# Kernel tuning notes

Hardware: AMD Instinct MI355X
Metric: run time of the kernel (lower is better)

## Reference

```python
import jax, jax.numpy as jnp
import numpy as np

N = 50000
E = 1600000
IN_DIM = 128
HID = 32
CLS = 40
HEADS = [4, 4, 1]
SLOPE = 0.2


def gat_conv(x, W, al, ar, src, dst, activation):
    # x: [N, F_in], W: [F_in, H*D], al/ar: [H, D]
    H, D = al.shape
    f = (x @ W).reshape(N, H, D)                       # projected features [N,H,D]
    el = jnp.sum(f * al, axis=-1)                      # [N,H]
    er = jnp.sum(f * ar, axis=-1)                      # [N,H]
    e = jax.nn.leaky_relu(el[src] + er[dst], SLOPE)    # [E,H] raw attention logits
    m = jax.ops.segment_max(e, dst, num_segments=N)    # per-dst max for stability
    m = jnp.where(jnp.isfinite(m), m, 0.0)
    ee = jnp.exp(e - m[dst])                           # [E,H]
    s = jax.ops.segment_sum(ee, dst, num_segments=N)   # [N,H]
    alpha = ee / s[dst]                                # edge softmax over in-neighbors
    out = jax.ops.segment_sum(alpha[..., None] * f[src], dst, num_segments=N)  # [N,H,D]
    if activation:
        out = jax.nn.elu(out)
    return out


def setup_inputs() -> dict:
    key = jax.random.key(0)
    ks = jax.random.split(key, 12)
    inputs = jax.random.normal(ks[0], (N, IN_DIM), dtype=jnp.float32)
    # random edges + self-loops so every node has >=1 in-edge
    src = jax.random.randint(ks[1], (E - N,), 0, N)
    dst = jax.random.randint(ks[2], (E - N,), 0, N)
    loops = jnp.arange(N)
    src = jnp.concatenate([src, loops])
    dst = jnp.concatenate([dst, loops])

    def glorot(k, shape):
        fan = shape[0] + shape[-1] * (shape[1] if len(shape) == 3 else 1)
        return jax.random.normal(k, shape, dtype=jnp.float32) * np.sqrt(2.0 / fan)

    W0 = glorot(ks[3], (IN_DIM, HEADS[0] * HID))
    al0 = jax.random.normal(ks[4], (HEADS[0], HID), dtype=jnp.float32) * 0.1
    ar0 = jax.random.normal(ks[5], (HEADS[0], HID), dtype=jnp.float32) * 0.1
    W1 = glorot(ks[6], (HEADS[0] * HID, HEADS[1] * HID))
    al1 = jax.random.normal(ks[7], (HEADS[1], HID), dtype=jnp.float32) * 0.1
    ar1 = jax.random.normal(ks[8], (HEADS[1], HID), dtype=jnp.float32) * 0.1
    W2 = glorot(ks[9], (HEADS[1] * HID, HEADS[2] * CLS))
    al2 = jax.random.normal(ks[10], (HEADS[2], CLS), dtype=jnp.float32) * 0.1
    ar2 = jax.random.normal(ks[11], (HEADS[2], CLS), dtype=jnp.float32) * 0.1
    return {"inputs": inputs, "src": src, "dst": dst,
            "W0": W0, "al0": al0, "ar0": ar0,
            "W1": W1, "al1": al1, "ar1": ar1,
            "W2": W2, "al2": al2, "ar2": ar2}


def reference(inputs, src, dst, W0, al0, ar0, W1, al1, ar1, W2, al2, ar2):
    h = gat_conv(inputs, W0, al0, ar0, src, dst, True).reshape(N, -1)   # flatten heads
    h = gat_conv(h, W1, al1, ar1, src, dst, True).reshape(N, -1)
    logits = gat_conv(h, W2, al2, ar2, src, dst, False).mean(axis=1)    # [N, CLS]
    return jax.nn.log_softmax(logits, axis=-1), h
```

## Files before the change

kernel.cpp:

```cpp
#include <hip/hip_runtime.h>
#include <hip/hip_fp16.h>
#include <math.h>

#define NN 50000
#define EE 1600000
#define DEGPAD 96
#define NWIN 200
#define WINSZ 250
#define WCAP 8960
#define BLDT 512
#define AGG_WPB 4

typedef _Float16 f16x8 __attribute__((ext_vector_type(8)));
typedef _Float16 f16x4v __attribute__((ext_vector_type(4)));
typedef _Float16 f16x2 __attribute__((ext_vector_type(2)));
typedef float f32x4 __attribute__((ext_vector_type(4)));
typedef float f32x2 __attribute__((ext_vector_type(2)));


__global__ void csr_clear(int* __restrict__ bcnt) {
    int i = blockIdx.x * blockDim.x + threadIdx.x;
    if (i < NWIN) bcnt[i] = 0;
}

__global__ void edge_bucket(const int* __restrict__ src, const int* __restrict__ dst,
                            int* __restrict__ bcnt, unsigned int* __restrict__ buck) {
    __shared__ int lcnt[NWIN];
    __shared__ int lbase[NWIN];
    int t = threadIdx.x;
    for (int i = t; i < NWIN; i += 256) lcnt[i] = 0;
    __syncthreads();
    unsigned int packs[8]; short wins[8]; short ranks[8];
    int e0 = blockIdx.x * 2048;
    #pragma unroll
    for (int it = 0; it < 8; ++it) {
        int e = e0 + it * 256 + t;
        wins[it] = -1;
        if (e < EE) {
            int d = dst[e], s = src[e];
            int w = d / WINSZ;
            wins[it] = (short)w;
            packs[it] = ((unsigned int)d << 16) | (unsigned int)s;
            ranks[it] = (short)atomicAdd(&lcnt[w], 1);
        }
    }
    __syncthreads();
    for (int i = t; i < NWIN; i += 256) lbase[i] = atomicAdd(&bcnt[i], lcnt[i]);
    __syncthreads();
    #pragma unroll
    for (int it = 0; it < 8; ++it) {
        if (wins[it] >= 0)
            buck[(int)wins[it] * WCAP + lbase[wins[it]] + (int)ranks[it]] = packs[it];
    }
}

__global__ void csr_build(const unsigned int* __restrict__ buck, const int* __restrict__ bcnt,
                          int* __restrict__ deg, unsigned short* __restrict__ csr16) {
    __shared__ unsigned short lcsr[WINSZ * DEGPAD];
    __shared__ int ldeg[WINSZ];
    int w = blockIdx.x;
    int n0 = w * WINSZ;
    int t = threadIdx.x;
    for (int i = t; i < WINSZ; i += BLDT) ldeg[i] = 0;
    __syncthreads();
    int cnt = bcnt[w];
    const unsigned int* b = buck + (size_t)w * WCAP;
    for (int i = t; i < cnt; i += BLDT) {
        unsigned int p = b[i];
        int d = (int)(p >> 16) - n0;
        int r = atomicAdd(&ldeg[d], 1);
        lcsr[d * DEGPAD + r] = (unsigned short)(p & 0xffffu);
    }
    __syncthreads();
    const int4* s4 = (const int4*)lcsr;
    int4* d4 = (int4*)(csr16 + (size_t)n0 * DEGPAD);
    for (int i = t; i < WINSZ * DEGPAD * 2 / 16; i += BLDT) d4[i] = s4[i];
    for (int i = t; i < WINSZ; i += BLDT) deg[n0 + i] = ldeg[i];
}


__global__ void cast_x(const float* __restrict__ x, _Float16* __restrict__ y) {
    int i = blockIdx.x * blockDim.x + threadIdx.x;
    if (i >= NN * 32) return;
    float4 v = ((const float4*)x)[i];
    f16x4v o;
    o.x = (_Float16)v.x; o.y = (_Float16)v.y; o.z = (_Float16)v.z; o.w = (_Float16)v.w;
    ((f16x4v*)y)[i] = o;
}

template<int CT, int CPAD, int CREAL, int HH, int CTPH, int F8>
__global__ void proj_mfma(const _Float16* __restrict__ x, const float* __restrict__ W,
                          const float* __restrict__ al, const float* __restrict__ ar,
                          void* __restrict__ fout, float* __restrict__ el,
                          float* __restrict__ er) {
    __shared__ _Float16 wl[4][CT][64][8];
    int lane = threadIdx.x & 63;
    int wave = threadIdx.x >> 6;
    int mrow = blockIdx.x * 64 + wave * 16;

    for (int slot = threadIdx.x; slot < 4 * CT * 64; slot += 256) {
        int lane_s = slot & 63;
        int ct = (slot >> 6) % CT;
        int ks = (slot >> 6) / CT;
        int k0 = ks * 32 + ((lane_s >> 4) << 3);
        int c = ct * 16 + (lane_s & 15);
        f16x8 v;
        #pragma unroll
        for (int j = 0; j < 8; ++j) {
            float w = (c < CREAL) ? W[(k0 + j) * CREAL + c] : 0.0f;
            v[j] = (_Float16)w;
        }
        *(f16x8*)(&wl[ks][ct][lane_s][0]) = v;
    }
    __syncthreads();

    const _Float16* xrow = x + (size_t)(mrow + (lane & 15)) * 128 + ((lane >> 4) << 3);
    f16x8 a[4];
    #pragma unroll
    for (int ks = 0; ks < 4; ++ks) a[ks] = *(const f16x8*)(xrow + ks * 32);

    f32x4 acc[CT];
    #pragma unroll
    for (int ct = 0; ct < CT; ++ct) acc[ct] = (f32x4){0.f, 0.f, 0.f, 0.f};

    #pragma unroll
    for (int ct = 0; ct < CT; ++ct) {
        #pragma unroll
        for (int ks = 0; ks < 4; ++ks) {
            f16x8 b = *(const f16x8*)(&wl[ks][ct][lane][0]);
            acc[ct] = __builtin_amdgcn_mfma_f32_16x16x32_f16(a[ks], b, acc[ct], 0, 0, 0);
        }
    }

    int colb = lane & 15;
    int rowg = lane >> 4;

    #pragma unroll
    for (int ct = 0; ct < CT; ++ct) {
        int c = ct * 16 + colb;
        #pragma unroll
        for (int j = 0; j < 4; ++j) {
            int r = rowg * 4 + j;
            if (F8) {
                int pk = __builtin_amdgcn_cvt_pk_fp8_f32(acc[ct][j], 0.0f, 0, false);
                ((unsigned char*)fout)[(size_t)(mrow + r) * CPAD + c] = (unsigned char)pk;
            } else {
                ((_Float16*)fout)[(size_t)(mrow + r) * CPAD + c] = (_Float16)acc[ct][j];
            }
        }
    }

    #pragma unroll
    for (int h = 0; h < HH; ++h) {
        float pl[4] = {0.f, 0.f, 0.f, 0.f};
        float pr[4] = {0.f, 0.f, 0.f, 0.f};
        #pragma unroll
        for (int q = 0; q < CTPH; ++q) {
            int ct = h * CTPH + q;
            int c = ct * 16 + colb;
            float av = (c < CREAL) ? al[c] : 0.0f;
            float rv = (c < CREAL) ? ar[c] : 0.0f;
            #pragma unroll
            for (int j = 0; j < 4; ++j) { pl[j] += acc[ct][j] * av; pr[j] += acc[ct][j] * rv; }
        }
        #pragma unroll
        for (int m = 1; m < 16; m <<= 1) {
            #pragma unroll
            for (int j = 0; j < 4; ++j) {
                pl[j] += __shfl_xor(pl[j], m);
                pr[j] += __shfl_xor(pr[j], m);
            }
        }
        if (colb == 0) {
            #pragma unroll
            for (int j = 0; j < 4; ++j) {
                int r = rowg * 4 + j;
                el[(size_t)(mrow + r) * HH + h] = pl[j];
                er[(size_t)(mrow + r) * HH + h] = pr[j];
            }
        }
    }
}

__global__ void agg128_kernel(const int* __restrict__ deg, const unsigned short* __restrict__ csr16,
                              const float* __restrict__ el, const float* __restrict__ er,
                              const unsigned char* __restrict__ f8, _Float16* __restrict__ out16,
                              float* __restrict__ out32) {
    __shared__ float ebuf_all[AGG_WPB][16][8];
    int wid  = threadIdx.x >> 6;
    int lane = threadIdx.x & 63;
    int n = blockIdx.x * AGG_WPB + wid;
    if (n >= NN) return;
    float (*ebuf)[8] = ebuf_all[wid];

    int start = n * DEGPAD, end = start + deg[n];
    int slot = lane >> 2, hh = lane & 3;
    int h = lane >> 4;
    float erh = er[n * 4 + hh];
    float acc0 = 0.f, acc1 = 0.f, s_part = 0.f;
    const unsigned char* fbase = f8 + (lane << 1);

    for (int base = start; base < end; base += 16) {
        int cnt = end - base; if (cnt > 16) cnt = 16;
        float eev = 0.0f; int snv = 0;
        if (slot < cnt) {
            snv = csr16[base + slot];
            float v = el[snv * 4 + hh] + erh;
            v = v > 0.0f ? v : 0.2f * v;
            eev = __expf(v);
        }
        s_part += eev;
        asm volatile("s_waitcnt lgkmcnt(0)" ::: "memory");
        ebuf[slot][2 * hh]     = eev;
        ebuf[slot][2 * hh + 1] = __int_as_float(snv);
        asm volatile("s_waitcnt lgkmcnt(0)" ::: "memory");
        #pragma unroll
        for (int g = 0; g < 2; ++g) {
            float ee[8]; int sn[8];
            #pragma unroll
            for (int q = 0; q < 8; ++q) {
                float2 p = *(const float2*)&ebuf[g * 8 + q][2 * h];
                ee[q] = p.x; sn[q] = __float_as_int(p.y);
            }
            unsigned short raw[8];
            #pragma unroll
            for (int q = 0; q < 8; ++q)
                raw[q] = *(const unsigned short*)(fbase + ((size_t)sn[q] << 7));
            #pragma unroll
            for (int q = 0; q < 8; ++q) {
                f32x2 fv = __builtin_amdgcn_cvt_pk_f32_fp8((int)raw[q], false);
                acc0 += ee[q] * fv[0];
                acc1 += ee[q] * fv[1];
            }
        }
    }
    #pragma unroll
    for (int m = 4; m < 64; m <<= 1) s_part += __shfl_xor(s_part, m);
    float sacc = __shfl(s_part, h);

    float o0 = acc0 / sacc, o1 = acc1 / sacc;
    float e0 = o0 > 0.f ? o0 : expm1f(o0);
    float e1 = o1 > 0.f ? o1 : expm1f(o1);
    f16x2 st; st[0] = (_Float16)e0; st[1] = (_Float16)e1;
    *(f16x2*)(out16 + (size_t)n * 128 + (lane << 1)) = st;
    if (out32) {
        float2 s2; s2.x = e0; s2.y = e1;
        *(float2*)(out32 + (size_t)n * 128 + (lane << 1)) = s2;
    }
}

__global__ void agg40_logsm_kernel(const int* __restrict__ deg, const unsigned short* __restrict__ csr16,
                                   const float* __restrict__ el, const float* __restrict__ er,
                                   const __half* __restrict__ f, float* __restrict__ out) {
    int n = blockIdx.x;
    int t = threadIdx.x;
    int start = n * DEGPAD, end = start + deg[n];
    float ern = er[n];
    __shared__ float eebuf[64];
    __shared__ int snbuf[64];

    float acc = 0.0f, sacc = 0.0f;
    for (int base = start; base < end; base += 64) {
        int cnt = end - base;
        if (cnt > 64) cnt = 64;
        if (t < cnt) {
            int sn = csr16[base + t];
            snbuf[t] = sn;
            float v = el[sn] + ern;
            v = v > 0.0f ? v : 0.2f * v;
            eebuf[t] = __expf(v);
        }
        __syncthreads();
        int j = 0;
        for (; j + 8 <= cnt; j += 8) {
            float ee[8]; int sn[8]; float fv[8];
            #pragma unroll
            for (int q = 0; q < 8; ++q) { ee[q] = eebuf[j + q]; sn[q] = snbuf[j + q]; }
            if (t < 40) {
                #pragma unroll
                for (int q = 0; q < 8; ++q) fv[q] = __half2float(f[((size_t)sn[q] << 6) + t]);
                #pragma unroll
                for (int q = 0; q < 8; ++q) acc += ee[q] * fv[q];
            }
            #pragma unroll
            for (int q = 0; q < 8; ++q) sacc += ee[q];
        }
        for (; j < cnt; ++j) {
            float ee = eebuf[j];
            sacc += ee;
            if (t < 40) acc += ee * __half2float(f[((size_t)snbuf[j] << 6) + t]);
        }
        __syncthreads();
    }
    float logit = (t < 40) ? acc / sacc : -INFINITY;

    float mx = logit;
    #pragma unroll
    for (int o = 32; o > 0; o >>= 1) mx = fmaxf(mx, __shfl_xor(mx, o));
    float ex = (t < 40) ? __expf(logit - mx) : 0.0f;
    float sm = ex;
    #pragma unroll
    for (int o = 32; o > 0; o >>= 1) sm += __shfl_xor(sm, o);
    if (t < 40) out[n * 40 + t] = logit - mx - logf(sm);
}


extern "C" void kernel_launch(void* const* d_in, const int* in_sizes, int n_in,
                              void* d_out, int out_size, void* d_ws, size_t ws_size,
                              hipStream_t stream) {
    const float* x0  = (const float*)d_in[0];
    const int*   src = (const int*)d_in[1];
    const int*   dst = (const int*)d_in[2];
    const float* W0  = (const float*)d_in[3];
    const float* al0 = (const float*)d_in[4];
    const float* ar0 = (const float*)d_in[5];
    const float* W1  = (const float*)d_in[6];
    const float* al1 = (const float*)d_in[7];
    const float* ar1 = (const float*)d_in[8];
    const float* W2  = (const float*)d_in[9];
    const float* al2 = (const float*)d_in[10];
    const float* ar2 = (const float*)d_in[11];

    float* out = (float*)d_out;
    char*  ws  = (char*)d_ws;

    int*            deg   = (int*)ws;
    int*            bcnt  = (int*)(ws + 200192);
    unsigned short* csr16 = (unsigned short*)(ws + 201216);
    unsigned int*   buck  = (unsigned int*)(ws + 9810432);
    unsigned char*  f8    = (unsigned char*)(ws + 16978432);
    _Float16*       f16a  = (_Float16*)(ws + 23384576);
    _Float16*       x16   = (_Float16*)(ws + 29790720);
    float*          el    = (float*)(ws + 42603008);
    float*          er    = (float*)(ws + 43403776);

    float* logsm = out;
    float* h1    = out + 2000000;

    const int PB = (NN + 63) / 64;
    const int AB = (NN + AGG_WPB - 1) / AGG_WPB;

    csr_clear  <<<1, 256, 0, stream>>>(bcnt);
    edge_bucket<<<(EE + 2047) / 2048, 256, 0, stream>>>(src, dst, bcnt, buck);
    csr_build  <<<NWIN, BLDT, 0, stream>>>(buck, bcnt, deg, csr16);

    cast_x<<<(NN * 32 + 255) / 256, 256, 0, stream>>>(x0, x16);
    proj_mfma<8, 128, 128, 4, 2, 1><<<PB, 256, 0, stream>>>(x16, W0, al0, ar0, f8, el, er);
    agg128_kernel<<<AB, 256, 0, stream>>>(deg, csr16, el, er, f8,
                                          x16, nullptr);

    proj_mfma<8, 128, 128, 4, 2, 1><<<PB, 256, 0, stream>>>(x16, W1, al1, ar1, f8, el, er);
    agg128_kernel<<<AB, 256, 0, stream>>>(deg, csr16, el, er, f8,
                                          x16, h1);

    proj_mfma<3, 64, 40, 1, 3, 0><<<PB, 256, 0, stream>>>(x16, W2, al2, ar2, f16a, el, er);
    agg40_logsm_kernel<<<NN, 64, 0, stream>>>(deg, csr16, el, er, (const __half*)f16a, logsm);
}
```

Measured before the change: 216.0 us.

## Store final-layer features as fp8 and aggregate one node per wavefront

The last-layer projection now writes fp8 features instead of fp16, matching the first two layers. The logits aggregation kernel is restructured to process four nodes per 256-thread block, one wavefront per node, instead of one 64-thread block per node. Edge weights and source ids are staged in per-wave shared memory and read with fixed waitcnt fences rather than __syncthreads. The inner loop is fully unrolled over all 64 slots, with zero weights for padding lanes. This is meant to halve gather bytes and cut launch and barrier overhead, at the cost of lower precision in the final logits and wasted work on padded slots for low-degree nodes.

```diff
diff --git a/kernel.cpp b/kernel.cpp
--- a/kernel.cpp
+++ b/kernel.cpp
@@ -251,57 +251,66 @@
 
 __global__ void agg40_logsm_kernel(const int* __restrict__ deg, const unsigned short* __restrict__ csr16,
                                    const float* __restrict__ el, const float* __restrict__ er,
-                                   const __half* __restrict__ f, float* __restrict__ out) {
-    int n = blockIdx.x;
-    int t = threadIdx.x;
+                                   const unsigned char* __restrict__ f8, float* __restrict__ out) {
+    __shared__ float ebuf_all[AGG_WPB][16][8];
+    int wid  = threadIdx.x >> 6;
+    int lane = threadIdx.x & 63;
+    int n = blockIdx.x * AGG_WPB + wid;
+    if (n >= NN) return;
+    float* ebuf = &ebuf_all[wid][0][0];
+
     int start = n * DEGPAD, end = start + deg[n];
     float ern = er[n];
-    __shared__ float eebuf[64];
-    __shared__ int snbuf[64];
-
-    float acc = 0.0f, sacc = 0.0f;
+    float acc = 0.0f, s_part = 0.0f;
+
     for (int base = start; base < end; base += 64) {
-        int cnt = end - base;
-        if (cnt > 64) cnt = 64;
-        if (t < cnt) {
-            int sn = csr16[base + t];
-            snbuf[t] = sn;
-            float v = el[sn] + ern;
+        int cnt = end - base; if (cnt > 64) cnt = 64;
+        float eev = 0.0f; int snv = 0;
+        if (lane < cnt) {
+            snv = csr16[base + lane];
+            float v = el[snv] + ern;
             v = v > 0.0f ? v : 0.2f * v;
-            eebuf[t] = __expf(v);
-        }
-        __syncthreads();
-        int j = 0;
-        for (; j + 8 <= cnt; j += 8) {
-            float ee[8]; int sn[8]; float fv[8];
-            #pragma unroll
-            for (int q = 0; q < 8; ++q) { ee[q] = eebuf[j + q]; sn[q] = snbuf[j + q]; }
-            if (t < 40) {
+            eev = __expf(v);
+        }
+        s_part += eev;
+        asm volatile("s_waitcnt lgkmcnt(0)" ::: "memory");
+        ebuf[2 * lane]     = eev;
+        ebuf[2 * lane + 1] = __int_as_float(snv);
+        asm volatile("s_waitcnt lgkmcnt(0)" ::: "memory");
+        #pragma unroll
+        for (int g = 0; g < 8; ++g) {
+            float ee[8]; int sn[8];
+            #pragma unroll
+            for (int q = 0; q < 8; ++q) {
+                float2 p = *(const float2*)(ebuf + 2 * (g * 8 + q));
+                ee[q] = p.x; sn[q] = __float_as_int(p.y);
+            }
+            if (lane < 40) {
+                unsigned char raw[8];
                 #pragma unroll
-                for (int q = 0; q < 8; ++q) fv[q] = __half2float(f[((size_t)sn[q] << 6) + t]);
+                for (int q = 0; q < 8; ++q)
+                    raw[q] = f8[((size_t)sn[q] << 6) + lane];
                 #pragma unroll
-                for (int q = 0; q < 8; ++q) acc += ee[q] * fv[q];
-            }
-            #pragma unroll
-            for (int q = 0; q < 8; ++q) sacc += ee[q];
-        }
-        for (; j < cnt; ++j) {
-            float ee = eebuf[j];
-            sacc += ee;
-            if (t < 40) acc += ee * __half2float(f[((size_t)snbuf[j] << 6) + t]);
-        }
-        __syncthreads();
-    }
-    float logit = (t < 40) ? acc / sacc : -INFINITY;
+                for (int q = 0; q < 8; ++q) {
+                    f32x2 fv = __builtin_amdgcn_cvt_pk_f32_fp8((int)raw[q], false);
+                    acc += ee[q] * fv[0];
+                }
+            }
+        }
+    }
+    #pragma unroll
+    for (int m = 1; m < 64; m <<= 1) s_part += __shfl_xor(s_part, m);
+
+    float logit = (lane < 40) ? acc / s_part : -INFINITY;
 
     float mx = logit;
     #pragma unroll
     for (int o = 32; o > 0; o >>= 1) mx = fmaxf(mx, __shfl_xor(mx, o));
-    float ex = (t < 40) ? __expf(logit - mx) : 0.0f;
+    float ex = (lane < 40) ? __expf(logit - mx) : 0.0f;
     float sm = ex;
     #pragma unroll
     for (int o = 32; o > 0; o >>= 1) sm += __shfl_xor(sm, o);
-    if (t < 40) out[n * 40 + t] = logit - mx - logf(sm);
+    if (lane < 40) out[(size_t)n * 40 + lane] = logit - mx - logf(sm);
 }
 
 
@@ -329,7 +338,7 @@
     unsigned short* csr16 = (unsigned short*)(ws + 201216);
     unsigned int*   buck  = (unsigned int*)(ws + 9810432);
     unsigned char*  f8    = (unsigned char*)(ws + 16978432);
-    _Float16*       f16a  = (_Float16*)(ws + 23384576);
+    unsigned char*  f8b   = (unsigned char*)(ws + 23384576);
     _Float16*       x16   = (_Float16*)(ws + 29790720);
     float*          el    = (float*)(ws + 42603008);
     float*          er    = (float*)(ws + 43403776);
@@ -353,6 +362,6 @@
     agg128_kernel<<<AB, 256, 0, stream>>>(deg, csr16, el, er, f8,
                                           x16, h1);
 
-    proj_mfma<3, 64, 40, 1, 3, 0><<<PB, 256, 0, stream>>>(x16, W2, al2, ar2, f16a, el, er);
-    agg40_logsm_kernel<<<NN, 64, 0, stream>>>(deg, csr16, el, er, (const __half*)f16a, logsm);
-}
+    proj_mfma<3, 64, 40, 1, 3, 1><<<PB, 256, 0, stream>>>(x16, W2, al2, ar2, f8b, el, er);
+    agg40_logsm_kernel<<<AB, 256, 0, stream>>>(deg, csr16, el, er, f8b, logsm);
+}
```

Result: slower. 224.2 us (+3.8%).
